# Kernel optimization log

Hardware: AMD Instinct MI355X
Metric: run time of the kernel (lower is better)

The kernel has to match this reference:

```python
import jax, jax.numpy as jnp
import numpy as np

N_QUBITS = 12
N_LAYERS = 4
BATCH = 4096
OUT_DIM = 12


def _ry(theta):
    theta = jnp.asarray(theta, jnp.float32)
    c, s = jnp.cos(theta / 2), jnp.sin(theta / 2)
    U = jnp.stack([jnp.stack([c, -s], -1), jnp.stack([s, c], -1)], -2)
    return U.astype(jnp.complex64)


def _rx(theta):
    theta = jnp.asarray(theta, jnp.float32)
    c = jnp.cos(theta / 2).astype(jnp.complex64)
    s = (-1j) * jnp.sin(theta / 2).astype(jnp.complex64)
    return jnp.stack([jnp.stack([c, s], -1), jnp.stack([s, c], -1)], -2)


def _rz(theta):
    theta = jnp.asarray(theta, jnp.float32)
    e = jnp.exp((-0.5j) * theta.astype(jnp.complex64))
    z = jnp.zeros_like(e)
    return jnp.stack([jnp.stack([e, z], -1), jnp.stack([z, jnp.conj(e)], -1)], -2)


def _apply_1q(psi, U, w):
    # psi: (B,) + (2,)*n; U: (2,2) shared gate or (B,2,2) per-sample gate
    psi = jnp.moveaxis(psi, w + 1, 1)
    if U.ndim == 2:
        psi = jnp.einsum('ij,bj...->bi...', U, psi)
    else:
        psi = jnp.einsum('bij,bj...->bi...', U, psi)
    return jnp.moveaxis(psi, 1, w + 1)


def _cnot(psi, c, t):
    # flip target axis where control bit == 1
    psi = jnp.moveaxis(psi, (c + 1, t + 1), (1, 2))
    psi = psi.at[:, 1].set(psi[:, 1, ::-1])
    return jnp.moveaxis(psi, (1, 2), (c + 1, t + 1))


def _pauli_z_signs(n):
    idx = np.arange(2 ** n)
    bits = (idx[None, :] >> (n - 1 - np.arange(n))[:, None]) & 1  # wire 0 = MSB
    return jnp.asarray(1.0 - 2.0 * bits, jnp.float32)  # (n, 2^n)


def _quantum_forward(x, quantum_weights):
    b, n = x.shape[0], N_QUBITS
    # tf.nn.l2_normalize(sample, axis=0) per sample
    xn = x * jax.lax.rsqrt(jnp.maximum(jnp.sum(x * x, axis=1, keepdims=True), 1e-12))
    # angle encoding: pi * x / (max|x| + 1e-8)
    angles = jnp.pi * xn / (jnp.max(jnp.abs(xn), axis=1, keepdims=True) + 1e-8)
    psi = jnp.zeros((b, 2 ** n), jnp.complex64).at[:, 0].set(1.0)
    psi = psi.reshape((b,) + (2,) * n)
    # data encoding: RY(angles[i]) on wire i (per-sample batched gates)
    for i in range(n):
        psi = _apply_1q(psi, _ry(angles[:, i]), i)
    # variational layers: RX/RY/RZ per qubit, then CNOT ring
    for layer in range(N_LAYERS):
        base = layer * 3 * n
        for i in range(n):
            p = base + 3 * i
            psi = _apply_1q(psi, _rx(quantum_weights[p]), i)
            psi = _apply_1q(psi, _ry(quantum_weights[p + 1]), i)
            psi = _apply_1q(psi, _rz(quantum_weights[p + 2]), i)
        for i in range(n):
            psi = _cnot(psi, i, (i + 1) % n)
    psi = psi.reshape(b, -1)
    probs = jnp.real(psi) ** 2 + jnp.imag(psi) ** 2  # (B, 2^n)
    return probs @ _pauli_z_signs(n).T  # (B, n): <Z_i> per qubit


def setup_inputs() -> dict:
    key = jax.random.key(0)
    k1, k2, k3 = jax.random.split(key, 3)
    n_params = 3 * N_QUBITS * N_LAYERS
    return {
        'x': jax.random.normal(k1, (BATCH, N_QUBITS), jnp.float32),
        'quantum_weights': jax.random.uniform(k2, (n_params,), jnp.float32, -0.05, 0.05),
        'dense_w': jax.random.normal(k3, (N_QUBITS, OUT_DIM), jnp.float32) / np.sqrt(N_QUBITS),
        'dense_b': jnp.zeros((OUT_DIM,), jnp.float32),
    }


def reference(x, quantum_weights, dense_w, dense_b):
    q = _quantum_forward(x, quantum_weights)
    return jnp.tanh(q @ dense_w + dense_b)
```

## Files before the change

### kernel.cpp

```cpp
#include <hip/hip_runtime.h>
#include <math.h>

#define NQ   12
#define NL   4
#define BLK  256
#define S1OFF 8192

typedef float v4f  __attribute__((ext_vector_type(4)));
typedef __fp16 v8h __attribute__((ext_vector_type(8)));

__device__ __forceinline__ constexpr int sigma_inv_c(int i) {
    int j = i;
    for (int c = 0; c < NQ; ++c) {
        int t = (c + 1) % NQ;
        int cb = (j >> (NQ - 1 - c)) & 1;
        j ^= cb << (NQ - 1 - t);
    }
    return j;
}

__device__ __forceinline__ constexpr int lswz(int l) {
    return l ^ (((l >> 3) ^ (l >> 7)) & 7);
}

__device__ __forceinline__ unsigned pk2(float a, float b) {
    return __builtin_bit_cast(unsigned, __builtin_amdgcn_cvt_pkrtz(a, b));
}

__device__ __forceinline__ int fslot(int k, int n) {
    return ((k >> 3) * 16 + n) * 8 + (k & 7);
}

__global__ __launch_bounds__(BLK) void gate_kernel(
    const float* __restrict__ qw, __fp16* __restrict__ gout)
{
    __shared__ float G[NQ][8];
    const int t = threadIdx.x;
    const int mat = blockIdx.x;
    const int layer = mat / 3, ph = mat - 3 * layer;
    if (t < NQ) {
        const int p = layer * 3 * NQ + 3 * t;
        float t1 = qw[p], t2 = qw[p + 1], t3 = qw[p + 2];
        float a, b, c, d, gr, h;
        sincosf(0.5f * t1, &b, &a);
        sincosf(0.5f * t2, &d, &c);
        sincosf(0.5f * t3, &h, &gr);
        float m00r =  c * a, m00i =  d * b;
        float m01r = -d * a, m01i = -c * b;
        float m10r =  d * a, m10i = -c * b;
        float m11r =  c * a, m11i = -d * b;
        float* g = G[t];
        g[0] = gr * m00r + h * m00i;  g[1] = gr * m00i - h * m00r;
        g[2] = gr * m01r + h * m01i;  g[3] = gr * m01i - h * m01r;
        g[4] = gr * m10r - h * m10i;  g[5] = gr * m10i + h * m10r;
        g[6] = gr * m11r - h * m11i;  g[7] = gr * m11i + h * m11r;
    }
    __syncthreads();
    const int n = t & 15, r = t >> 4;
    const int wbase = (ph == 0) ? 8 : (ph == 1) ? 4 : 0;
    float cr = 1.f, ci = 0.f;
    #pragma unroll
    for (int b = 0; b < 4; ++b) {
        const float* g = G[wbase + b];
        const int rb = (r >> (3 - b)) & 1, nb = (n >> (3 - b)) & 1;
        const float er = g[(nb * 2 + rb) * 2], ei = g[(nb * 2 + rb) * 2 + 1];
        const float xr = cr * er - ci * ei, xi = cr * ei + ci * er;
        cr = xr; ci = xi;
    }
    __fp16* b1 = gout + (mat * 2 + 0) * 512;
    __fp16* b2 = gout + (mat * 2 + 1) * 512;
    b1[fslot(2 * r, n)]     = (__fp16)cr;
    b1[fslot(2 * r + 1, n)] = (__fp16)(-ci);
    b2[fslot(2 * r, n)]     = (__fp16)ci;
    b2[fslot(2 * r + 1, n)] = (__fp16)cr;
}

#define READ_FRAGS(AF, SRC)                                                 \
    _Pragma("unroll")                                                       \
    for (int q = 0; q < 4; ++q)                                             \
        AF[q] = __builtin_bit_cast(v8h, *(const uint4*)&sh[(SRC) +          \
                    lswz((((wv) << 6) | (q << 4) | nn) * 4 + g) * 8]);

#define BLOAD(MAT)                                                          \
    const v8h b1 = gf[((MAT) * 2 + 0) * 64 + lane];                         \
    const v8h b2 = gf[((MAT) * 2 + 1) * 64 + lane];

#define MFMA_ONE(AF)                                                        \
    _Pragma("unroll")                                                       \
    for (int q = 0; q < 4; ++q) {                                           \
        d1[q] = __builtin_amdgcn_mfma_f32_16x16x32_f16(AF[q], b1, zf, 0, 0, 0); \
        d2[q] = __builtin_amdgcn_mfma_f32_16x16x32_f16(AF[q], b2, zf, 0, 0, 0); \
    }

#define SCHB __builtin_amdgcn_sched_barrier(0);

#define WRITE_COLS(DST)                                                     \
    _Pragma("unroll")                                                       \
    for (int q = 0; q < 4; ++q) {                                           \
        const int CCn = (nn << 4) | (wv << 2) | q;                          \
        *(uint4*)&sh[(DST) + lswz(CCn * 4 + g) * 8] =                       \
            make_uint4(pk2(d1[q].x, d2[q].x), pk2(d1[q].y, d2[q].y),        \
                       pk2(d1[q].z, d2[q].z), pk2(d1[q].w, d2[q].w));       \
    }

#define WRITE_SIGMA(DST)                                                    \
    _Pragma("unroll")                                                       \
    for (int q = 0; q < 4; ++q) {                                           \
        const int iq = ifix ^ sigma_inv_c(q << 4);                          \
        _Pragma("unroll")                                                   \
        for (int rg = 0; rg < 4; ++rg) {                                    \
            const int ii = iq ^ sigma_inv_c(rg);                            \
            *(unsigned*)&sh[(DST) + lswz(ii >> 2) * 8 + (ii & 3) * 2] =     \
                pk2(d1[q][rg], d2[q][rg]);                                  \
        }                                                                   \
    }

#define WHT_VALS(VALS)                                                      \
    { float pr[16];                                                         \
      _Pragma("unroll")                                                     \
      for (int q = 0; q < 4; ++q)                                           \
          _Pragma("unroll")                                                 \
          for (int rg = 0; rg < 4; ++rg)                                    \
              pr[q * 4 + rg] = d1[q][rg] * d1[q][rg] + d2[q][rg] * d2[q][rg]; \
      _Pragma("unroll")                                                     \
      for (int st = 1; st < 16; st <<= 1) {                                 \
          _Pragma("unroll")                                                 \
          for (int i = 0; i < 16; ++i) {                                    \
              if (!(i & st)) {                                              \
                  const float a = pr[i], b = pr[i ^ st];                    \
                  pr[i] = a + b; pr[i ^ st] = a - b;                        \
              }                                                             \
          }                                                                 \
      }                                                                     \
      _Pragma("unroll")                                                     \
      for (int w = 0; w < NQ; ++w) {                                        \
          const int sb = 11 - w;                                            \
          const int f = (((sigma_inv_c(0x20) >> sb) & 1) << 3)              \
                      | (((sigma_inv_c(0x10) >> sb) & 1) << 2)              \
                      | (((sigma_inv_c(2)    >> sb) & 1) << 1)              \
                      |  ((sigma_inv_c(1)    >> sb) & 1);                   \
          const float v = pr[f];                                            \
          VALS[w] = ((ifix >> sb) & 1) ? -v : v;                            \
      } }

__global__ __launch_bounds__(BLK) void qsim_kernel(
    const float* __restrict__ x,
    const __fp16* __restrict__ gates,
    const float* __restrict__ dw,
    const float* __restrict__ db,
    float* __restrict__ out,
    int batch)
{
    __shared__ __align__(16) __fp16 sh[16384];
    float* xv    = (float*)sh;
    float* enc_c = (float*)sh + 32;
    float* enc_s = (float*)sh + 64;
    float* red   = (float*)sh;

    const int tid  = threadIdx.x;
    const int lane = tid & 63;
    const int wv   = tid >> 6;
    const int s0   = 2 * blockIdx.x;
    int s1 = s0 + 1; if (s1 >= batch) s1 = batch - 1;
    const int nn = lane & 15, g = lane >> 4;
    const v8h* gf = (const v8h*)gates;
    const v4f zf = {0.f, 0.f, 0.f, 0.f};

    if (tid < 2 * NQ) {
        const int smp = tid / NQ, j = tid - smp * NQ;
        xv[tid] = x[(smp ? s1 : s0) * NQ + j];
    }
    __syncthreads();
    if (tid < 2 * NQ) {
        const int base = (tid / NQ) * NQ;
        float ss = 0.f;
        #pragma unroll
        for (int j = 0; j < NQ; ++j) ss += xv[base + j] * xv[base + j];
        float inv = rsqrtf(fmaxf(ss, 1e-12f));
        float mx = 0.f;
        #pragma unroll
        for (int j = 0; j < NQ; ++j) mx = fmaxf(mx, fabsf(xv[base + j] * inv));
        float ang = 3.14159265358979323846f * (xv[tid] * inv) / (mx + 1e-8f);
        float cc, sn;
        sincosf(0.5f * ang, &sn, &cc);
        enc_c[tid] = cc; enc_s[tid] = sn;
    }
    __syncthreads();

    v8h af0[4], af1[4];
    #define PICK(SMP, W, B) ((B) ? enc_s[(SMP) * NQ + (W)] : enc_c[(SMP) * NQ + (W)])
    #define INIT_AF(AF, SMP)                                                \
    {   float R4[4];                                                        \
        _Pragma("unroll")                                                   \
        for (int t = 0; t < 4; ++t) {                                       \
            const int r = 4 * g + t;                                        \
            R4[t] = PICK(SMP, 8, (r >> 3) & 1) * PICK(SMP, 9, (r >> 2) & 1) \
                  * PICK(SMP, 10, (r >> 1) & 1) * PICK(SMP, 11, r & 1);     \
        }                                                                   \
        const float Pfix = PICK(SMP, 0, (wv >> 1) & 1) * PICK(SMP, 1, wv & 1) \
                         * PICK(SMP, 4, (nn >> 3) & 1) * PICK(SMP, 5, (nn >> 2) & 1) \
                         * PICK(SMP, 6, (nn >> 1) & 1) * PICK(SMP, 7, nn & 1); \
        _Pragma("unroll")                                                   \
        for (int q = 0; q < 4; ++q) {                                       \
            const float Pq = Pfix * PICK(SMP, 2, (q >> 1) & 1) * PICK(SMP, 3, q & 1); \
            _Pragma("unroll")                                               \
            for (int t = 0; t < 4; ++t) {                                   \
                AF[q][2 * t]     = (__fp16)(Pq * R4[t]);                    \
                AF[q][2 * t + 1] = (__fp16)0.f;                             \
            }                                                               \
        }                                                                   \
    }
    INIT_AF(af0, 0)
    INIT_AF(af1, 1)
    #undef PICK
    __syncthreads();

    const int ifix = sigma_inv_c((nn << 8) | (wv << 6) | (g << 2));

    v4f d1[4], d2[4];
    float vals0[NQ], vals1[NQ];
    #pragma unroll 1
    for (int l = 0; l < NL; ++l) {
        if (l > 0) {
            READ_FRAGS(af0, 0)
            READ_FRAGS(af1, S1OFF)
            __syncthreads();
        }
        { BLOAD(l * 3 + 0)
          MFMA_ONE(af0) WRITE_COLS(0)
          SCHB
          MFMA_ONE(af1) WRITE_COLS(S1OFF) }
        __syncthreads();

        READ_FRAGS(af0, 0)
        READ_FRAGS(af1, S1OFF)
        __syncthreads();
        { BLOAD(l * 3 + 1)
          MFMA_ONE(af0) WRITE_COLS(0)
          SCHB
          MFMA_ONE(af1) WRITE_COLS(S1OFF) }
        __syncthreads();

        READ_FRAGS(af0, 0)
        READ_FRAGS(af1, S1OFF)
        if (l < NL - 1) {
            __syncthreads();
            { BLOAD(l * 3 + 2)
              MFMA_ONE(af0) WRITE_SIGMA(0)
              SCHB
              MFMA_ONE(af1) WRITE_SIGMA(S1OFF) }
            __syncthreads();
        } else {
            { BLOAD(l * 3 + 2)
              MFMA_ONE(af0)
              WHT_VALS(vals0)
              SCHB
              MFMA_ONE(af1)
              WHT_VALS(vals1) }
        }
    }

    #pragma unroll
    for (int m = 1; m <= 32; m <<= 1) {
        #pragma unroll
        for (int w = 0; w < NQ; ++w) {
            vals0[w] += __shfl_xor(vals0[w], m);
            vals1[w] += __shfl_xor(vals1[w], m);
        }
    }
    __syncthreads();
    if (lane == 0) {
        #pragma unroll
        for (int w = 0; w < NQ; ++w) {
            red[wv * NQ + w]      = vals0[w];
            red[48 + wv * NQ + w] = vals1[w];
        }
    }
    __syncthreads();
    if (tid < 2 * NQ) {
        const int smp = tid / NQ, w = tid - smp * NQ;
        const float* rs = red + smp * 48;
        red[96 + tid] = rs[w] + rs[NQ + w] + rs[2 * NQ + w] + rs[3 * NQ + w];
    }
    __syncthreads();
    if (tid < 2 * NQ) {
        const int smp = tid / NQ, o = tid - smp * NQ;
        const float* rv = red + 96 + smp * NQ;
        float v = db[o];
        #pragma unroll
        for (int w = 0; w < NQ; ++w) v += rv[w] * dw[w * NQ + o];
        out[(smp ? s1 : s0) * NQ + o] = tanhf(v);
    }
}

extern "C" void kernel_launch(void* const* d_in, const int* in_sizes, int n_in,
                              void* d_out, int out_size, void* d_ws, size_t ws_size,
                              hipStream_t stream) {
    const float* x  = (const float*)d_in[0];
    const float* qw = (const float*)d_in[1];
    const float* dw = (const float*)d_in[2];
    const float* db = (const float*)d_in[3];
    float* out = (float*)d_out;
    __fp16* gates = (__fp16*)d_ws;
    int batch = in_sizes[0] / NQ;
    int nblk = (batch + 1) / 2;
    gate_kernel<<<12, BLK, 0, stream>>>(qw, gates);
    qsim_kernel<<<nblk, BLK, 0, stream>>>(x, gates, dw, db, out, batch);
}
```

Baseline: 114.7 us.

## Split qsim work across 8 waves per block with per-half MFMA fragments

Doubles the qsim block to 512 threads so each wave handles half of the previous four fragment columns. This halves per-thread register use for fragments and accumulators, aiming at more waves in flight. The final Walsh-Hadamard epilogue is cut to 8 points, with a qh-dependent sign. Its reduction now does a 16-lane shuffle and writes partial sums to shared memory, followed by a 32-way sum. The cost is more barrier participants per block and an extra sync before the last layer.

```diff
diff --git a/kernel.cpp b/kernel.cpp
--- a/kernel.cpp
+++ b/kernel.cpp
@@ -3,7 +3,8 @@
 
 #define NQ   12
 #define NL   4
-#define BLK  256
+#define GBLK 256
+#define QBLK 512
 #define S1OFF 8192
 
 typedef float v4f  __attribute__((ext_vector_type(4)));
@@ -31,7 +32,7 @@
     return ((k >> 3) * 16 + n) * 8 + (k & 7);
 }
 
-__global__ __launch_bounds__(BLK) void gate_kernel(
+__global__ __launch_bounds__(GBLK) void gate_kernel(
     const float* __restrict__ qw, __fp16* __restrict__ gout)
 {
     __shared__ float G[NQ][8];
@@ -77,9 +78,9 @@
 
 #define READ_FRAGS(AF, SRC)                                                 \
     _Pragma("unroll")                                                       \
-    for (int q = 0; q < 4; ++q)                                             \
-        AF[q] = __builtin_bit_cast(v8h, *(const uint4*)&sh[(SRC) +          \
-                    lswz((((wv) << 6) | (q << 4) | nn) * 4 + g) * 8]);
+    for (int j = 0; j < 2; ++j)                                             \
+        AF[j] = __builtin_bit_cast(v8h, *(const uint4*)&sh[(SRC) +          \
+                    lswz((((wv) << 6) | ((2 * qh + j) << 4) | nn) * 4 + g) * 8]);
 
 #define BLOAD(MAT)                                                          \
     const v8h b1 = gf[((MAT) * 2 + 0) * 64 + lane];                         \
@@ -87,63 +88,75 @@
 
 #define MFMA_ONE(AF)                                                        \
     _Pragma("unroll")                                                       \
-    for (int q = 0; q < 4; ++q) {                                           \
-        d1[q] = __builtin_amdgcn_mfma_f32_16x16x32_f16(AF[q], b1, zf, 0, 0, 0); \
-        d2[q] = __builtin_amdgcn_mfma_f32_16x16x32_f16(AF[q], b2, zf, 0, 0, 0); \
+    for (int j = 0; j < 2; ++j) {                                           \
+        d1[j] = __builtin_amdgcn_mfma_f32_16x16x32_f16(AF[j], b1, zf, 0, 0, 0); \
+        d2[j] = __builtin_amdgcn_mfma_f32_16x16x32_f16(AF[j], b2, zf, 0, 0, 0); \
     }
 
 #define SCHB __builtin_amdgcn_sched_barrier(0);
 
 #define WRITE_COLS(DST)                                                     \
     _Pragma("unroll")                                                       \
-    for (int q = 0; q < 4; ++q) {                                           \
-        const int CCn = (nn << 4) | (wv << 2) | q;                          \
+    for (int j = 0; j < 2; ++j) {                                           \
+        const int CCn = (nn << 4) | (wv << 2) | (2 * qh + j);               \
         *(uint4*)&sh[(DST) + lswz(CCn * 4 + g) * 8] =                       \
-            make_uint4(pk2(d1[q].x, d2[q].x), pk2(d1[q].y, d2[q].y),        \
-                       pk2(d1[q].z, d2[q].z), pk2(d1[q].w, d2[q].w));       \
+            make_uint4(pk2(d1[j].x, d2[j].x), pk2(d1[j].y, d2[j].y),        \
+                       pk2(d1[j].z, d2[j].z), pk2(d1[j].w, d2[j].w));       \
     }
 
 #define WRITE_SIGMA(DST)                                                    \
     _Pragma("unroll")                                                       \
-    for (int q = 0; q < 4; ++q) {                                           \
-        const int iq = ifix ^ sigma_inv_c(q << 4);                          \
+    for (int j = 0; j < 2; ++j) {                                           \
+        const int iq = ifix ^ (j ? sq1 : sq0);                              \
         _Pragma("unroll")                                                   \
         for (int rg = 0; rg < 4; ++rg) {                                    \
             const int ii = iq ^ sigma_inv_c(rg);                            \
             *(unsigned*)&sh[(DST) + lswz(ii >> 2) * 8 + (ii & 3) * 2] =     \
-                pk2(d1[q][rg], d2[q][rg]);                                  \
+                pk2(d1[j][rg], d2[j][rg]);                                  \
         }                                                                   \
     }
 
-#define WHT_VALS(VALS)                                                      \
-    { float pr[16];                                                         \
+#define WHT_EPI(OFF)                                                        \
+    { float p8[8];                                                          \
       _Pragma("unroll")                                                     \
-      for (int q = 0; q < 4; ++q)                                           \
+      for (int j = 0; j < 2; ++j)                                           \
           _Pragma("unroll")                                                 \
           for (int rg = 0; rg < 4; ++rg)                                    \
-              pr[q * 4 + rg] = d1[q][rg] * d1[q][rg] + d2[q][rg] * d2[q][rg]; \
+              p8[j * 4 + rg] = d1[j][rg] * d1[j][rg] + d2[j][rg] * d2[j][rg]; \
       _Pragma("unroll")                                                     \
-      for (int st = 1; st < 16; st <<= 1) {                                 \
+      for (int st = 1; st < 8; st <<= 1) {                                  \
           _Pragma("unroll")                                                 \
-          for (int i = 0; i < 16; ++i) {                                    \
+          for (int i = 0; i < 8; ++i) {                                     \
               if (!(i & st)) {                                              \
-                  const float a = pr[i], b = pr[i ^ st];                    \
-                  pr[i] = a + b; pr[i ^ st] = a - b;                        \
+                  const float a = p8[i], b = p8[i ^ st];                    \
+                  p8[i] = a + b; p8[i ^ st] = a - b;                        \
               }                                                             \
           }                                                                 \
       }                                                                     \
+      float vals[NQ];                                                       \
       _Pragma("unroll")                                                     \
       for (int w = 0; w < NQ; ++w) {                                        \
           const int sb = 11 - w;                                            \
-          const int f = (((sigma_inv_c(0x20) >> sb) & 1) << 3)              \
-                      | (((sigma_inv_c(0x10) >> sb) & 1) << 2)              \
-                      | (((sigma_inv_c(2)    >> sb) & 1) << 1)              \
-                      |  ((sigma_inv_c(1)    >> sb) & 1);                   \
-          const float v = pr[f];                                            \
-          VALS[w] = ((ifix >> sb) & 1) ? -v : v;                            \
+          const int f3 = (sigma_inv_c(0x20) >> sb) & 1;                     \
+          const int f2 = (sigma_inv_c(0x10) >> sb) & 1;                     \
+          const int f1 = (sigma_inv_c(2)    >> sb) & 1;                     \
+          const int f0 = (sigma_inv_c(1)    >> sb) & 1;                     \
+          const float v = p8[f2 * 4 + f1 * 2 + f0];                         \
+          const int sgn = ((ifix >> sb) & 1) ^ (f3 & qh);                   \
+          vals[w] = sgn ? -v : v;                                           \
+      }                                                                     \
+      _Pragma("unroll")                                                     \
+      for (int m = 1; m <= 8; m <<= 1) {                                    \
+          _Pragma("unroll")                                                 \
+          for (int w = 0; w < NQ; ++w) vals[w] += __shfl_xor(vals[w], m);   \
+      }                                                                     \
+      if ((lane & 15) == 0) {                                               \
+          _Pragma("unroll")                                                 \
+          for (int w = 0; w < NQ; ++w)                                      \
+              red[(OFF) + W * 48 + (lane >> 4) * 12 + w] = vals[w];         \
       } }
 
-__global__ __launch_bounds__(BLK) void qsim_kernel(
+__global__ __launch_bounds__(QBLK, 8) void qsim_kernel(
     const float* __restrict__ x,
     const __fp16* __restrict__ gates,
     const float* __restrict__ dw,
@@ -159,7 +172,9 @@
 
     const int tid  = threadIdx.x;
     const int lane = tid & 63;
-    const int wv   = tid >> 6;
+    const int W    = tid >> 6;
+    const int wv   = W & 3;
+    const int qh   = W >> 2;
     const int s0   = 2 * blockIdx.x;
     int s1 = s0 + 1; if (s1 >= batch) s1 = batch - 1;
     const int nn = lane & 15, g = lane >> 4;
@@ -187,8 +202,8 @@
     }
     __syncthreads();
 
-    v8h af0[4], af1[4];
-    #define PICK(SMP, W, B) ((B) ? enc_s[(SMP) * NQ + (W)] : enc_c[(SMP) * NQ + (W)])
+    v8h af0[2], af1[2];
+    #define PICK(SMP, WW, B) ((B) ? enc_s[(SMP) * NQ + (WW)] : enc_c[(SMP) * NQ + (WW)])
     #define INIT_AF(AF, SMP)                                                \
     {   float R4[4];                                                        \
         _Pragma("unroll")                                                   \
@@ -201,12 +216,12 @@
                          * PICK(SMP, 4, (nn >> 3) & 1) * PICK(SMP, 5, (nn >> 2) & 1) \
                          * PICK(SMP, 6, (nn >> 1) & 1) * PICK(SMP, 7, nn & 1); \
         _Pragma("unroll")                                                   \
-        for (int q = 0; q < 4; ++q) {                                       \
-            const float Pq = Pfix * PICK(SMP, 2, (q >> 1) & 1) * PICK(SMP, 3, q & 1); \
+        for (int j = 0; j < 2; ++j) {                                       \
+            const float Pq = Pfix * PICK(SMP, 2, qh) * PICK(SMP, 3, j);     \
             _Pragma("unroll")                                               \
             for (int t = 0; t < 4; ++t) {                                   \
-                AF[q][2 * t]     = (__fp16)(Pq * R4[t]);                    \
-                AF[q][2 * t + 1] = (__fp16)0.f;                             \
+                AF[j][2 * t]     = (__fp16)(Pq * R4[t]);                    \
+                AF[j][2 * t + 1] = (__fp16)0.f;                             \
             }                                                               \
         }                                                                   \
     }
@@ -216,9 +231,10 @@
     __syncthreads();
 
     const int ifix = sigma_inv_c((nn << 8) | (wv << 6) | (g << 2));
-
-    v4f d1[4], d2[4];
-    float vals0[NQ], vals1[NQ];
+    const int sq0 = qh ? sigma_inv_c(0x20) : 0;
+    const int sq1 = qh ? sigma_inv_c(0x30) : sigma_inv_c(0x10);
+
+    v4f d1[2], d2[2];
     #pragma unroll 1
     for (int l = 0; l < NL; ++l) {
         if (l > 0) {
@@ -243,8 +259,8 @@
 
         READ_FRAGS(af0, 0)
         READ_FRAGS(af1, S1OFF)
+        __syncthreads();
         if (l < NL - 1) {
-            __syncthreads();
             { BLOAD(l * 3 + 2)
               MFMA_ONE(af0) WRITE_SIGMA(0)
               SCHB
@@ -253,39 +269,25 @@
         } else {
             { BLOAD(l * 3 + 2)
               MFMA_ONE(af0)
-              WHT_VALS(vals0)
+              WHT_EPI(0)
               SCHB
               MFMA_ONE(af1)
-              WHT_VALS(vals1) }
+              WHT_EPI(384) }
         }
     }
 
-    #pragma unroll
-    for (int m = 1; m <= 32; m <<= 1) {
-        #pragma unroll
-        for (int w = 0; w < NQ; ++w) {
-            vals0[w] += __shfl_xor(vals0[w], m);
-            vals1[w] += __shfl_xor(vals1[w], m);
-        }
-    }
-    __syncthreads();
-    if (lane == 0) {
-        #pragma unroll
-        for (int w = 0; w < NQ; ++w) {
-            red[wv * NQ + w]      = vals0[w];
-            red[48 + wv * NQ + w] = vals1[w];
-        }
-    }
     __syncthreads();
     if (tid < 2 * NQ) {
         const int smp = tid / NQ, w = tid - smp * NQ;
-        const float* rs = red + smp * 48;
-        red[96 + tid] = rs[w] + rs[NQ + w] + rs[2 * NQ + w] + rs[3 * NQ + w];
+        float acc = 0.f;
+        #pragma unroll
+        for (int k = 0; k < 32; ++k) acc += red[smp * 384 + k * 12 + w];
+        red[768 + tid] = acc;
     }
     __syncthreads();
     if (tid < 2 * NQ) {
         const int smp = tid / NQ, o = tid - smp * NQ;
-        const float* rv = red + 96 + smp * NQ;
+        const float* rv = red + 768 + smp * NQ;
         float v = db[o];
         #pragma unroll
         for (int w = 0; w < NQ; ++w) v += rv[w] * dw[w * NQ + o];
@@ -304,6 +306,6 @@
     __fp16* gates = (__fp16*)d_ws;
     int batch = in_sizes[0] / NQ;
     int nblk = (batch + 1) / 2;
-    gate_kernel<<<12, BLK, 0, stream>>>(qw, gates);
-    qsim_kernel<<<nblk, BLK, 0, stream>>>(x, gates, dw, db, out, batch);
-}
+    gate_kernel<<<12, GBLK, 0, stream>>>(qw, gates);
+    qsim_kernel<<<nblk, QBLK, 0, stream>>>(x, gates, dw, db, out, batch);
+}
```

Result: slower. 123.7 us (+7.8%).
